# Optimization experiments

Hardware: AMD Instinct MI355X
Metric: run time of the kernel (lower is better)

## Reference

```python
import jax, jax.numpy as jnp
import numpy as np

B, N, M, D, H, F = 2, 2048, 2048, 512, 8, 2048
EPS = 1e-6


def _ln(x, g, b):
    mu = x.mean(-1, keepdims=True)
    var = ((x - mu) ** 2).mean(-1, keepdims=True)
    return (x - mu) / jnp.sqrt(var + EPS) * g + b


def setup_inputs() -> dict:
    key = jax.random.key(0)
    ks = jax.random.split(key, 12)
    g = lambda k, s: (jax.random.normal(k, s, jnp.float32) * 0.02)
    inp = {
        "x": jax.random.normal(ks[0], (B, N, D), jnp.float32),
        "y": jax.random.normal(ks[1], (B, M, D), jnp.float32),
        "mask_x": jnp.ones((B, N), jnp.float32),
        "mask_y": jnp.ones((B, M), jnp.float32),
        # MaskAttention params (weights stored as [in, out], applied as x @ W + b)
        "Wq": g(ks[2], (D, D)), "bq": jnp.zeros((D,), jnp.float32),
        "Wk": g(ks[3], (D, D)), "bk": jnp.zeros((D,), jnp.float32),
        "Wv": g(ks[4], (D, D)), "bv": jnp.zeros((D,), jnp.float32),
        "Wo": g(ks[5], (D, D)), "bo": jnp.zeros((D,), jnp.float32),
        # Mlp params
        "W1": g(ks[6], (D, F)), "b1": g(ks[7], (F,)) * 1e-4,
        "W2": g(ks[8], (F, D)), "b2": g(ks[9], (D,)) * 1e-4,
        # LayerNorm params (attention_norm shared between x and y; ffn_norm)
        "ln1_g": jnp.ones((D,), jnp.float32), "ln1_b": jnp.zeros((D,), jnp.float32),
        "ln2_g": jnp.ones((D,), jnp.float32), "ln2_b": jnp.zeros((D,), jnp.float32),
    }
    return inp


def reference(x, y, mask_x, mask_y, Wq, bq, Wk, bk, Wv, bv, Wo, bo,
              W1, b1, W2, b2, ln1_g, ln1_b, ln2_g, ln2_b):
    b, n, d = x.shape
    dh = d // H
    h = x
    xn = _ln(x, ln1_g, ln1_b)   # shared attention_norm
    yn = _ln(y, ln1_g, ln1_b)
    # masked Q/K/V projections (mask applied to mixed layers before head split)
    q = (xn @ Wq + bq) * mask_x[..., None]
    k = (yn @ Wk + bk) * mask_y[..., None]
    v = (yn @ Wv + bv) * mask_y[..., None]
    q = q.reshape(b, n, H, dh)
    k = k.reshape(b, -1, H, dh)
    v = v.reshape(b, -1, H, dh)
    scores = jnp.einsum("bnhd,bmhd->bhnm", q, k) / np.sqrt(dh)  # [B,H,N,M]
    probs = jax.nn.softmax(scores, axis=-1)
    ctx = jnp.einsum("bhnm,bmhd->bnhd", probs, v).reshape(b, n, d)
    attn_out = ctx @ Wo + bo  # proj_dropout is identity in eval
    x = h + attn_out
    h2 = x
    xn2 = _ln(x, ln2_g, ln2_b)
    ff = jax.nn.gelu(xn2 @ W1 + b1, approximate=False) @ W2 + b2
    return h2 + ff
```

## Files before the change

### kernel.cpp

```cpp
#include <hip/hip_runtime.h>
#include <hip/hip_bf16.h>

#define B_  2
#define N_  2048
#define M_  2048
#define D_  512
#define H_  8
#define F_  2048
#define DH_ 64
#define ROWS 4096

#define SPLIT 4
#define KV_PER (M_ / SPLIT)
#define NT (KV_PER / 64)

typedef __bf16 bf16x8 __attribute__((ext_vector_type(8)));
typedef __bf16 bf16x4v __attribute__((ext_vector_type(4)));
typedef float  f32x4  __attribute__((ext_vector_type(4)));
using bf16 = __hip_bfloat16;

__global__ __launch_bounds__(256) void ln_kernel(
    const float* __restrict__ in, const float* __restrict__ gam,
    const float* __restrict__ bet, bf16* __restrict__ out)
{
    int wave = threadIdx.x >> 6, lane = threadIdx.x & 63;
    int row  = blockIdx.x * 4 + wave;
    const float* p = in + (size_t)row * D_ + lane * 8;
    float4 v0 = *(const float4*)p;
    float4 v1 = *(const float4*)(p + 4);
    float s  = v0.x + v0.y + v0.z + v0.w + v1.x + v1.y + v1.z + v1.w;
    float ss = v0.x*v0.x + v0.y*v0.y + v0.z*v0.z + v0.w*v0.w
             + v1.x*v1.x + v1.y*v1.y + v1.z*v1.z + v1.w*v1.w;
    for (int m = 1; m < 64; m <<= 1) {
        s  += __shfl_xor(s,  m, 64);
        ss += __shfl_xor(ss, m, 64);
    }
    float mu   = s * (1.f / D_);
    float var  = ss * (1.f / D_) - mu * mu;
    float rstd = rsqrtf(var + 1e-6f);
    int c = lane * 8;
    float4 g0 = *(const float4*)(gam + c), g1 = *(const float4*)(gam + c + 4);
    float4 b0 = *(const float4*)(bet + c), b1 = *(const float4*)(bet + c + 4);
    bf16* o = out + (size_t)row * D_ + c;
    o[0] = __float2bfloat16((v0.x - mu) * rstd * g0.x + b0.x);
    o[1] = __float2bfloat16((v0.y - mu) * rstd * g0.y + b0.y);
    o[2] = __float2bfloat16((v0.z - mu) * rstd * g0.z + b0.z);
    o[3] = __float2bfloat16((v0.w - mu) * rstd * g0.w + b0.w);
    o[4] = __float2bfloat16((v1.x - mu) * rstd * g1.x + b1.x);
    o[5] = __float2bfloat16((v1.y - mu) * rstd * g1.y + b1.y);
    o[6] = __float2bfloat16((v1.z - mu) * rstd * g1.z + b1.z);
    o[7] = __float2bfloat16((v1.w - mu) * rstd * g1.w + b1.w);
}

__global__ void wtrans_kernel(const float* __restrict__ W, bf16* __restrict__ Wt,
                              int K, int N)
{
    __shared__ float t[32][33];
    int tx = threadIdx.x, ty = threadIdx.y;
    int n0 = blockIdx.x * 32, k0 = blockIdx.y * 32;
    for (int j = 0; j < 32; j += 8)
        t[ty + j][tx] = W[(size_t)(k0 + ty + j) * N + n0 + tx];
    __syncthreads();
    for (int j = 0; j < 32; j += 8)
        Wt[(size_t)(n0 + ty + j) * K + k0 + tx] = __float2bfloat16(t[tx][ty + j]);
}

__global__ void wtrans4_kernel(const float* __restrict__ Wq, const float* __restrict__ Wk,
                               const float* __restrict__ Wv, const float* __restrict__ Wo,
                               bf16* __restrict__ Wqt, bf16* __restrict__ Wkt,
                               bf16* __restrict__ Wvt, bf16* __restrict__ Wot)
{
    int z = blockIdx.z;
    const float* W = z == 0 ? Wq : (z == 1 ? Wk : (z == 2 ? Wv : Wo));
    bf16* Wt       = z == 0 ? Wqt : (z == 1 ? Wkt : (z == 2 ? Wvt : Wot));
    __shared__ float t[32][33];
    int tx = threadIdx.x, ty = threadIdx.y;
    int n0 = blockIdx.x * 32, k0 = blockIdx.y * 32;
    for (int j = 0; j < 32; j += 8)
        t[ty + j][tx] = W[(size_t)(k0 + ty + j) * D_ + n0 + tx];
    __syncthreads();
    for (int j = 0; j < 32; j += 8)
        Wt[(size_t)(n0 + ty + j) * D_ + k0 + tx] = __float2bfloat16(t[tx][ty + j]);
}

__global__ void vtrans_kernel(const bf16* __restrict__ v, bf16* __restrict__ vt)
{
    __shared__ bf16 t[32][33];
    int tx = threadIdx.x, ty = threadIdx.y;
    int bh = blockIdx.z, b = bh >> 3, h = bh & 7;
    int m0 = blockIdx.x * 32, d0 = blockIdx.y * 32;
    for (int j = 0; j < 32; j += 8)
        t[ty + j][tx] = v[(size_t)(b * M_ + m0 + ty + j) * D_ + h * DH_ + d0 + tx];
    __syncthreads();
    for (int j = 0; j < 32; j += 8)
        vt[((size_t)bh * DH_ + d0 + ty + j) * M_ + m0 + tx] = t[tx][ty + j];
}

#define BM 128
#define BN 128
#define BK 32
#define LDK 40

#define GEMM_BODY(Aptr, Btptr, KK, EPILOGUE)                                         \
    __shared__ bf16 As[BM * LDK];                                                    \
    __shared__ bf16 Bs[BN * LDK];                                                    \
    int t = threadIdx.x;                                                             \
    int lane = t & 63, wave = t >> 6;                                                \
    int wm = wave >> 1, wn = wave & 1;                                               \
    int r16 = lane & 15, g = lane >> 4;                                              \
    int m0 = blockIdx.x * BM, n0 = blockIdx.y * BN;                                  \
    f32x4 acc[4][4] = {};                                                            \
    for (int k0 = 0; k0 < (KK); k0 += BK) {                                          \
        __syncthreads();                                                             \
        for (int it = 0; it < 2; ++it) {                                             \
            int c = it * 256 + t;                                                    \
            int row = c >> 2, ko = (c & 3) * 8;                                      \
            uint4 dA = *(const uint4*)((Aptr)  + (size_t)(m0 + row) * (KK) + k0 + ko); \
            *(uint4*)((char*)As + row * (LDK * 2) + ko * 2) = dA;                    \
            uint4 dB = *(const uint4*)((Btptr) + (size_t)(n0 + row) * (KK) + k0 + ko); \
            *(uint4*)((char*)Bs + row * (LDK * 2) + ko * 2) = dB;                    \
        }                                                                            \
        __syncthreads();                                                             \
        bf16x8 af[4], bfr[4];                                                        \
        for (int i = 0; i < 4; ++i)                                                  \
            af[i]  = *(const bf16x8*)((char*)As + (wm * 64 + i * 16 + r16) * (LDK * 2) + g * 16); \
        for (int i = 0; i < 4; ++i)                                                  \
            bfr[i] = *(const bf16x8*)((char*)Bs + (wn * 64 + i * 16 + r16) * (LDK * 2) + g * 16); \
        for (int i = 0; i < 4; ++i)                                                  \
            for (int j = 0; j < 4; ++j)                                              \
                acc[i][j] = __builtin_amdgcn_mfma_f32_16x16x32_bf16(af[i], bfr[j], acc[i][j], 0, 0, 0); \
    }                                                                                \
    for (int i = 0; i < 4; ++i) {                                                    \
        int rb = m0 + wm * 64 + i * 16 + g * 4;                                      \
        for (int j = 0; j < 4; ++j) {                                                \
            int cb = n0 + wn * 64 + j * 16 + r16;                                    \
            float bia = bias[cb];                                                    \
            for (int e = 0; e < 4; ++e) {                                            \
                int rr = rb + e;                                                     \
                float val = acc[i][j][e] + bia;                                      \
                EPILOGUE                                                             \
            }                                                                        \
        }                                                                            \
    }

template<bool GELU, bool RESID, bool ROWMASK, bool OUTBF>
__global__ __launch_bounds__(256) void gemm_bt(
    const bf16* __restrict__ A, const bf16* __restrict__ Bt,
    const float* __restrict__ bias, const float* __restrict__ resid,
    const float* __restrict__ rowmask,
    bf16* __restrict__ outb, float* __restrict__ outf,
    int Mr, int Nn, int K)
{
    GEMM_BODY(A, Bt, K,
        if (GELU)    val = 0.5f * val * (1.f + erff(val * 0.70710678118654752f));
        if (RESID)   val += resid[(size_t)rr * Nn + cb];
        if (ROWMASK) val *= rowmask[rr];
        if (OUTBF)   outb[(size_t)rr * Nn + cb] = __float2bfloat16(val);
        else         outf[(size_t)rr * Nn + cb] = val;
    )
}

template<bool RESID, bool ROWMASK, bool OUTBF>
__device__ __forceinline__ void gemm64_body(
    const bf16* __restrict__ A, const bf16* __restrict__ Bt,
    const float* __restrict__ bias, const float* __restrict__ resid,
    const float* __restrict__ rowmask,
    bf16* __restrict__ outb, float* __restrict__ outf,
    int Nn, int K)
{
    __shared__ __align__(16) char As[2][64 * 128];
    __shared__ __align__(16) char Bs[2][64 * 128];
    int t = threadIdx.x, lane = t & 63, wave = t >> 6;
    int wm = wave >> 1, wn = wave & 1;
    int r16 = lane & 15, g = lane >> 4;
    int m0 = blockIdx.x * 64, n0 = blockIdx.y * 64;

    const int sr0 = t >> 3, sr1 = sr0 + 32, sc = t & 7;
    const int wof0 = sr0 * 128 + ((sc ^ (sr0 & 7)) << 4);
    const int wof1 = sr1 * 128 + ((sc ^ (sr1 & 7)) << 4);
    const int rsw0 = ((g     ^ (r16 & 7)) << 4);
    const int rsw1 = (((4 + g) ^ (r16 & 7)) << 4);

    uint4 a0, a1, b0, b1;
#define G64_LOAD(k0)                                                         \
    a0 = *(const uint4*)(A  + (size_t)(m0 + sr0) * K + (k0) + sc * 8);       \
    a1 = *(const uint4*)(A  + (size_t)(m0 + sr1) * K + (k0) + sc * 8);       \
    b0 = *(const uint4*)(Bt + (size_t)(n0 + sr0) * K + (k0) + sc * 8);       \
    b1 = *(const uint4*)(Bt + (size_t)(n0 + sr1) * K + (k0) + sc * 8);
#define G64_WRITE(buf)                                                       \
    *(uint4*)(As[buf] + wof0) = a0;  *(uint4*)(As[buf] + wof1) = a1;         \
    *(uint4*)(Bs[buf] + wof0) = b0;  *(uint4*)(Bs[buf] + wof1) = b1;

    f32x4 acc[2][2] = {};
    G64_LOAD(0)
    G64_WRITE(0)
    int cur = 0;
    const int nit = K >> 6;
    for (int it = 0; it < nit; ++it) {
        if (it + 1 < nit) { G64_LOAD((it + 1) << 6) }
        __syncthreads();
        bf16x8 af[2][2], bfr[2][2];
#pragma unroll
        for (int i = 0; i < 2; ++i) {
            af[i][0] = *(const bf16x8*)(As[cur] + (wm * 32 + i * 16 + r16) * 128 + rsw0);
            af[i][1] = *(const bf16x8*)(As[cur] + (wm * 32 + i * 16 + r16) * 128 + rsw1);
            bfr[i][0] = *(const bf16x8*)(Bs[cur] + (wn * 32 + i * 16 + r16) * 128 + rsw0);
            bfr[i][1] = *(const bf16x8*)(Bs[cur] + (wn * 32 + i * 16 + r16) * 128 + rsw1);
        }
        __builtin_amdgcn_s_setprio(1);
#pragma unroll
        for (int i = 0; i < 2; ++i)
#pragma unroll
            for (int j = 0; j < 2; ++j) {
                acc[i][j] = __builtin_amdgcn_mfma_f32_16x16x32_bf16(af[i][0], bfr[j][0], acc[i][j], 0, 0, 0);
                acc[i][j] = __builtin_amdgcn_mfma_f32_16x16x32_bf16(af[i][1], bfr[j][1], acc[i][j], 0, 0, 0);
            }
        __builtin_amdgcn_s_setprio(0);
        if (it + 1 < nit) { G64_WRITE(cur ^ 1) }
        cur ^= 1;
    }
#undef G64_LOAD
#undef G64_WRITE

#pragma unroll
    for (int i = 0; i < 2; ++i) {
        int rb = m0 + wm * 32 + i * 16 + g * 4;
#pragma unroll
        for (int j = 0; j < 2; ++j) {
            int cb = n0 + wn * 32 + j * 16 + r16;
            float bia = bias[cb];
#pragma unroll
            for (int e = 0; e < 4; ++e) {
                int rr = rb + e;
                float val = acc[i][j][e] + bia;
                if (RESID)   val += resid[(size_t)rr * Nn + cb];
                if (ROWMASK) val *= rowmask[rr];
                if (OUTBF)   outb[(size_t)rr * Nn + cb] = __float2bfloat16(val);
                else         outf[(size_t)rr * Nn + cb] = val;
            }
        }
    }
}

template<bool RESID, bool OUTBF>
__global__ __launch_bounds__(256) void gemm64(
    const bf16* __restrict__ A, const bf16* __restrict__ Bt,
    const float* __restrict__ bias, const float* __restrict__ resid,
    bf16* __restrict__ outb, float* __restrict__ outf, int Nn, int K)
{
    gemm64_body<RESID, false, OUTBF>(A, Bt, bias, resid, nullptr, outb, outf, Nn, K);
}

__global__ __launch_bounds__(256) void gemm64_qkv(
    const bf16* __restrict__ xn, const bf16* __restrict__ yn,
    const bf16* __restrict__ Wqt, const bf16* __restrict__ Wkt, const bf16* __restrict__ Wvt,
    const float* __restrict__ bq, const float* __restrict__ bk, const float* __restrict__ bv,
    const float* __restrict__ mask_x, const float* __restrict__ mask_y,
    bf16* __restrict__ qb, bf16* __restrict__ kb, bf16* __restrict__ vb)
{
    int z = blockIdx.z;
    const bf16* A        = z == 0 ? xn : yn;
    const bf16* Bt       = z == 0 ? Wqt : (z == 1 ? Wkt : Wvt);
    const float* bias    = z == 0 ? bq  : (z == 1 ? bk  : bv);
    const float* rowmask = z == 0 ? mask_x : mask_y;
    bf16* outb           = z == 0 ? qb  : (z == 1 ? kb  : vb);
    gemm64_body<false, true, true>(A, Bt, bias, nullptr, rowmask, outb, nullptr, D_, D_);
}

__global__ __launch_bounds__(256, 3) void attn_kernel(
    const bf16* __restrict__ q, const bf16* __restrict__ kk,
    const bf16* __restrict__ vt, float* __restrict__ num,
    float* __restrict__ ml)
{
    int bh = blockIdx.y, b = bh >> 3, h = bh & 7;
    int n0 = blockIdx.x * 128;
    int sp = blockIdx.z;
    int t = threadIdx.x, lane = t & 63, wave = t >> 6;
    int ql = lane & 15, gg = lane >> 4;

    __shared__ __align__(16) char KsB[2][64 * 128];
    __shared__ __align__(16) char VsB[2][64 * 128];
    __shared__ __align__(16) bf16 plds[4][16][72];

    bf16x8 qf0[2], qf1[2];
    {
        int qr0 = b * N_ + n0 + wave * 32 + ql;
        for (int ks = 0; ks < 2; ++ks) {
            bf16x8 qv = *(const bf16x8*)(q + (size_t)qr0 * D_ + h * DH_ + ks * 32 + gg * 8);
            for (int j = 0; j < 8; ++j) qv[j] = (__bf16)((float)qv[j] * 0.125f);
            qf0[ks] = qv;
            bf16x8 qw = *(const bf16x8*)(q + (size_t)(qr0 + 16) * D_ + h * DH_ + ks * 32 + gg * 8);
            for (int j = 0; j < 8; ++j) qw[j] = (__bf16)((float)qw[j] * 0.125f);
            qf1[ks] = qw;
        }
    }

    f32x4 cacc0[4] = {}, cacc1[4] = {};
    float m0r = -1e30f, l0r = 0.f, m1r = -1e30f, l1r = 0.f;

    const bf16* kbase = kk + (size_t)(b * M_ + sp * KV_PER) * D_ + h * DH_;
    const bf16* vtb   = vt + (size_t)bh * DH_ * M_ + sp * KV_PER;

    const int k0r = t >> 3,          kc0 = t & 7;
    const int k1r = (t >> 3) + 32;
    const int wofs0 = k0r * 128 + ((kc0 ^ (k0r & 7)) << 4);
    const int wofs1 = k1r * 128 + ((kc0 ^ (k1r & 7)) << 4);
    const int rsw0 = ((gg     ^ (ql & 7)) << 4);
    const int rsw1 = (((4 + gg) ^ (ql & 7)) << 4);

#define STAGE_LOAD(tt)                                                              \
    kw0 = *(const uint4*)(kbase + (size_t)((tt) * 64 + k0r) * D_ + kc0 * 8);        \
    kw1 = *(const uint4*)(kbase + (size_t)((tt) * 64 + k1r) * D_ + kc0 * 8);        \
    vw0 = *(const uint4*)(vtb + (size_t)k0r * M_ + (tt) * 64 + kc0 * 8);            \
    vw1 = *(const uint4*)(vtb + (size_t)k1r * M_ + (tt) * 64 + kc0 * 8);

#define STAGE_WRITE(buf)                                                            \
    *(uint4*)(KsB[buf] + wofs0) = kw0;                                              \
    *(uint4*)(KsB[buf] + wofs1) = kw1;                                              \
    *(uint4*)(VsB[buf] + wofs0) = vw0;                                              \
    *(uint4*)(VsB[buf] + wofs1) = vw1;

#define SOFTMAX_PV(S, MR, LR, CACC)                                                 \
    {                                                                               \
        float tmax = fmaxf(                                                         \
            fmaxf(fmaxf(fmaxf(S[0][0], S[0][1]), fmaxf(S[0][2], S[0][3])),          \
                  fmaxf(fmaxf(S[1][0], S[1][1]), fmaxf(S[1][2], S[1][3]))),         \
            fmaxf(fmaxf(fmaxf(S[2][0], S[2][1]), fmaxf(S[2][2], S[2][3])),          \
                  fmaxf(fmaxf(S[3][0], S[3][1]), fmaxf(S[3][2], S[3][3]))));        \
        tmax = fmaxf(tmax, __shfl_xor(tmax, 16, 64));                               \
        tmax = fmaxf(tmax, __shfl_xor(tmax, 32, 64));                               \
        float mnew = fmaxf(MR, tmax);                                               \
        float scl  = __expf(MR - mnew);                                             \
        MR = mnew;                                                                  \
        float p[4][4]; float ps = 0.f;                                              \
        for (int nf = 0; nf < 4; ++nf)                                              \
            for (int e = 0; e < 4; ++e) { p[nf][e] = __expf(S[nf][e] - mnew); ps += p[nf][e]; } \
        ps += __shfl_xor(ps, 16, 64);                                               \
        ps += __shfl_xor(ps, 32, 64);                                               \
        LR = LR * scl + ps;                                                         \
        for (int df = 0; df < 4; ++df)                                              \
            for (int e = 0; e < 4; ++e) CACC[df][e] *= scl;                         \
        for (int nf = 0; nf < 4; ++nf) {                                            \
            bf16x4v w;                                                              \
            w[0] = (__bf16)p[nf][0]; w[1] = (__bf16)p[nf][1];                       \
            w[2] = (__bf16)p[nf][2]; w[3] = (__bf16)p[nf][3];                       \
            *(bf16x4v*)(&plds[wave][ql][nf * 16 + 4 * gg]) = w;                     \
        }                                                                           \
        __builtin_amdgcn_s_setprio(1);                                              \
        for (int ks = 0; ks < 2; ++ks) {                                            \
            bf16x8 pf = *(const bf16x8*)((const char*)&plds[wave][0][0]             \
                                         + ql * 144 + ks * 64 + gg * 16);           \
            for (int df = 0; df < 4; ++df)                                          \
                CACC[df] = __builtin_amdgcn_mfma_f32_16x16x32_bf16(                 \
                    vf[df * 2 + ks], pf, CACC[df], 0, 0, 0);                        \
        }                                                                           \
        __builtin_amdgcn_s_setprio(0);                                              \
    }

    uint4 kw0, kw1, vw0, vw1;
    STAGE_LOAD(0)
    STAGE_WRITE(0)
    int cur = 0;

    for (int tt = 0; tt < NT; ++tt) {
        if (tt + 1 < NT) { STAGE_LOAD(tt + 1) }
        __syncthreads();

        const char* Kb = KsB[cur];
        const char* Vb = VsB[cur];

        bf16x8 kf[8];
#pragma unroll
        for (int nf = 0; nf < 4; ++nf) {
            kf[nf * 2 + 0] = *(const bf16x8*)(Kb + (nf * 16 + ql) * 128 + rsw0);
            kf[nf * 2 + 1] = *(const bf16x8*)(Kb + (nf * 16 + ql) * 128 + rsw1);
        }

        f32x4 s0[4] = {}, s1[4] = {};
        __builtin_amdgcn_s_setprio(1);
#pragma unroll
        for (int nf = 0; nf < 4; ++nf) {
            s0[nf] = __builtin_amdgcn_mfma_f32_16x16x32_bf16(kf[nf * 2 + 0], qf0[0], s0[nf], 0, 0, 0);
            s0[nf] = __builtin_amdgcn_mfma_f32_16x16x32_bf16(kf[nf * 2 + 1], qf0[1], s0[nf], 0, 0, 0);
            s1[nf] = __builtin_amdgcn_mfma_f32_16x16x32_bf16(kf[nf * 2 + 0], qf1[0], s1[nf], 0, 0, 0);
            s1[nf] = __builtin_amdgcn_mfma_f32_16x16x32_bf16(kf[nf * 2 + 1], qf1[1], s1[nf], 0, 0, 0);
        }
        __builtin_amdgcn_s_setprio(0);

        bf16x8 vf[8];
#pragma unroll
        for (int df = 0; df < 4; ++df) {
            vf[df * 2 + 0] = *(const bf16x8*)(Vb + (df * 16 + ql) * 128 + rsw0);
            vf[df * 2 + 1] = *(const bf16x8*)(Vb + (df * 16 + ql) * 128 + rsw1);
        }

        SOFTMAX_PV(s0, m0r, l0r, cacc0)
        SOFTMAX_PV(s1, m1r, l1r, cacc1)

        if (tt + 1 < NT) { STAGE_WRITE(cur ^ 1) }
        cur ^= 1;
    }

    {
        int qr0 = b * N_ + n0 + wave * 32 + ql;
        float* nb0 = num + (size_t)sp * ROWS * D_ + (size_t)qr0 * D_ + h * DH_;
        float* nb1 = num + (size_t)sp * ROWS * D_ + (size_t)(qr0 + 16) * D_ + h * DH_;
#pragma unroll
        for (int df = 0; df < 4; ++df) {
            *(f32x4*)(nb0 + df * 16 + 4 * gg) = cacc0[df];
            *(f32x4*)(nb1 + df * 16 + 4 * gg) = cacc1[df];
        }
        if (lane < 16) {
            size_t base = ((size_t)(sp * (B_ * H_) + bh) * N_ + (n0 + wave * 32 + ql)) * 2;
            ml[base] = m0r; ml[base + 1] = l0r;
            size_t base1 = ((size_t)(sp * (B_ * H_) + bh) * N_ + (n0 + wave * 32 + 16 + ql)) * 2;
            ml[base1] = m1r; ml[base1 + 1] = l1r;
        }
    }
#undef STAGE_LOAD
#undef STAGE_WRITE
#undef SOFTMAX_PV
}

__global__ __launch_bounds__(256) void attn_combine(
    const float* __restrict__ num, const float* __restrict__ ml,
    bf16* __restrict__ ctx)
{
    int idx = blockIdx.x * 256 + threadIdx.x;
    int row = idx >> 7;
    int c4  = (idx & 127) << 2;
    int b = row >> 11, n = row & (N_ - 1);
    int h = c4 >> 6;
    int bh = (b << 3) + h;
    float mv[SPLIT], lv[SPLIT];
#pragma unroll
    for (int sp = 0; sp < SPLIT; ++sp) {
        const float* mp = ml + ((size_t)(sp * (B_ * H_) + bh) * N_ + n) * 2;
        mv[sp] = mp[0]; lv[sp] = mp[1];
    }
    float mx = mv[0];
#pragma unroll
    for (int sp = 1; sp < SPLIT; ++sp) mx = fmaxf(mx, mv[sp]);
    float den = 0.f;
    float wsc[SPLIT];
#pragma unroll
    for (int sp = 0; sp < SPLIT; ++sp) {
        wsc[sp] = __expf(mv[sp] - mx);
        den += wsc[sp] * lv[sp];
    }
    float inv = 1.f / den;
    float ax = 0.f, ay = 0.f, az = 0.f, aw = 0.f;
#pragma unroll
    for (int sp = 0; sp < SPLIT; ++sp) {
        float4 v = *(const float4*)(num + (size_t)sp * ROWS * D_ + (size_t)row * D_ + c4);
        ax += wsc[sp] * v.x; ay += wsc[sp] * v.y;
        az += wsc[sp] * v.z; aw += wsc[sp] * v.w;
    }
    bf16* o = ctx + (size_t)row * D_ + c4;
    o[0] = __float2bfloat16(ax * inv);
    o[1] = __float2bfloat16(ay * inv);
    o[2] = __float2bfloat16(az * inv);
    o[3] = __float2bfloat16(aw * inv);
}

extern "C" void kernel_launch(void* const* d_in, const int* in_sizes, int n_in,
                              void* d_out, int out_size, void* d_ws, size_t ws_size,
                              hipStream_t stream)
{
    const float* x      = (const float*)d_in[0];
    const float* y      = (const float*)d_in[1];
    const float* mask_x = (const float*)d_in[2];
    const float* mask_y = (const float*)d_in[3];
    const float* Wq = (const float*)d_in[4];  const float* bq = (const float*)d_in[5];
    const float* Wk = (const float*)d_in[6];  const float* bk = (const float*)d_in[7];
    const float* Wv = (const float*)d_in[8];  const float* bv = (const float*)d_in[9];
    const float* Wo = (const float*)d_in[10]; const float* bo = (const float*)d_in[11];
    const float* W1 = (const float*)d_in[12]; const float* b1 = (const float*)d_in[13];
    const float* W2 = (const float*)d_in[14]; const float* b2 = (const float*)d_in[15];
    const float* ln1g = (const float*)d_in[16]; const float* ln1b = (const float*)d_in[17];
    const float* ln2g = (const float*)d_in[18]; const float* ln2b = (const float*)d_in[19];

    char* ws = (char*)d_ws;
    const size_t SZA = (size_t)ROWS * D_ * 2;
    bf16* xn   = (bf16*)ws;            ws += SZA;
    bf16* yn   = (bf16*)ws;            ws += SZA;
    bf16* qb   = (bf16*)ws;            ws += SZA;
    bf16* kb   = (bf16*)ws;            ws += SZA;
    bf16* vb   = (bf16*)ws;            ws += SZA;
    bf16* vtb  = (bf16*)ws;            ws += SZA;
    bf16* ctxb = (bf16*)ws;            ws += SZA;
    bf16* xn2  = (bf16*)ws;            ws += SZA;
    bf16* hff  = (bf16*)ws;            ws += (size_t)ROWS * F_ * 2;
    float* x1  = (float*)ws;           ws += (size_t)ROWS * D_ * 4;
    bf16* Wqt = (bf16*)ws;             ws += (size_t)D_ * D_ * 2;
    bf16* Wkt = (bf16*)ws;             ws += (size_t)D_ * D_ * 2;
    bf16* Wvt = (bf16*)ws;             ws += (size_t)D_ * D_ * 2;
    bf16* Wot = (bf16*)ws;             ws += (size_t)D_ * D_ * 2;
    bf16* W1t = (bf16*)ws;             ws += (size_t)D_ * F_ * 2;
    bf16* W2t = (bf16*)ws;             ws += (size_t)F_ * D_ * 2;
    float* num = (float*)ws;           ws += (size_t)SPLIT * ROWS * D_ * 4;
    float* mlb = (float*)ws;           ws += (size_t)SPLIT * B_ * H_ * N_ * 2 * 4;

    dim3 tb(32, 8);
    wtrans4_kernel<<<dim3(D_ / 32, D_ / 32, 4), tb, 0, stream>>>(
        Wq, Wk, Wv, Wo, Wqt, Wkt, Wvt, Wot);
    wtrans_kernel<<<dim3(F_ / 32, D_ / 32), tb, 0, stream>>>(W1, W1t, D_, F_);
    wtrans_kernel<<<dim3(D_ / 32, F_ / 32), tb, 0, stream>>>(W2, W2t, F_, D_);

    ln_kernel<<<ROWS / 4, 256, 0, stream>>>(x, ln1g, ln1b, xn);
    ln_kernel<<<ROWS / 4, 256, 0, stream>>>(y, ln1g, ln1b, yn);

    gemm64_qkv<<<dim3(ROWS / 64, D_ / 64, 3), 256, 0, stream>>>(
        xn, yn, Wqt, Wkt, Wvt, bq, bk, bv, mask_x, mask_y, qb, kb, vb);

    vtrans_kernel<<<dim3(M_ / 32, DH_ / 32, B_ * H_), tb, 0, stream>>>(vb, vtb);

    attn_kernel<<<dim3(N_ / 128, B_ * H_, SPLIT), 256, 0, stream>>>(qb, kb, vtb, num, mlb);
    attn_combine<<<(ROWS * D_ / 4) / 256, 256, 0, stream>>>(num, mlb, ctxb);

    gemm64<true, false><<<dim3(ROWS / 64, D_ / 64), 256, 0, stream>>>(
        ctxb, Wot, bo, x, nullptr, x1, D_, D_);

    ln_kernel<<<ROWS / 4, 256, 0, stream>>>(x1, ln2g, ln2b, xn2);

    gemm_bt<true, false, false, true><<<dim3(ROWS / BM, F_ / BN), 256, 0, stream>>>(
        xn2, W1t, b1, nullptr, nullptr, hff, nullptr, ROWS, F_, D_);

    gemm64<true, false><<<dim3(ROWS / 64, D_ / 64), 256, 0, stream>>>(
        hff, W2t, b2, x1, nullptr, (float*)d_out, D_, F_);
}
```

Baseline: 137.1 us.

## Halve attention split, remap grid for XCD locality, lazy rescale, bf16 partials

Reduces the KV split from 4 to 2 and flattens the attention grid to 1D, remapping block IDs so consecutive blocks are spread across the 8 XCDs in a locality-friendly order. The online softmax now rescales the accumulator and running max only when some lane's tile max exceeds the stored max by more than 8, skipping the exp and multiplies in most iterations. Partial numerators are stored as bf16 instead of fp32, halving combine traffic. The risks are less parallelism with fewer splits, an extra rounding step on the partials, and probabilities that can exceed 1 (up to e^8) before normalisation, which loosens precision.

```diff
diff --git a/kernel.cpp b/kernel.cpp
--- a/kernel.cpp
+++ b/kernel.cpp
@@ -10,9 +10,10 @@
 #define DH_ 64
 #define ROWS 4096
 
-#define SPLIT 4
+#define SPLIT 2
 #define KV_PER (M_ / SPLIT)
 #define NT (KV_PER / 64)
+#define ATT_GRID (16 * 16 * SPLIT)
 
 typedef __bf16 bf16x8 __attribute__((ext_vector_type(8)));
 typedef __bf16 bf16x4v __attribute__((ext_vector_type(4)));
@@ -269,12 +270,15 @@
 
 __global__ __launch_bounds__(256, 3) void attn_kernel(
     const bf16* __restrict__ q, const bf16* __restrict__ kk,
-    const bf16* __restrict__ vt, float* __restrict__ num,
+    const bf16* __restrict__ vt, bf16* __restrict__ num,
     float* __restrict__ ml)
 {
-    int bh = blockIdx.y, b = bh >> 3, h = bh & 7;
-    int n0 = blockIdx.x * 128;
-    int sp = blockIdx.z;
+    int bid = blockIdx.x;
+    int wg  = (bid & 7) * (ATT_GRID / 8) + (bid >> 3);
+    int n0  = (wg & 15) * 128;
+    int bh  = (wg >> 4) & 15;
+    int sp  = wg >> 8;
+    int b = bh >> 3, h = bh & 7;
     int t = threadIdx.x, lane = t & 63, wave = t >> 6;
     int ql = lane & 15, gg = lane >> 4;
 
@@ -329,17 +333,20 @@
                   fmaxf(fmaxf(S[3][0], S[3][1]), fmaxf(S[3][2], S[3][3]))));        \
         tmax = fmaxf(tmax, __shfl_xor(tmax, 16, 64));                               \
         tmax = fmaxf(tmax, __shfl_xor(tmax, 32, 64));                               \
-        float mnew = fmaxf(MR, tmax);                                               \
-        float scl  = __expf(MR - mnew);                                             \
-        MR = mnew;                                                                  \
+        if (__any(tmax - MR > 8.f)) {                     \
+            float mnew = fmaxf(MR, tmax);                                           \
+            float scl  = __expf(MR - mnew);                                         \
+            MR = mnew;                                                              \
+            LR *= scl;                                                              \
+            for (int df = 0; df < 4; ++df)                                          \
+                for (int e = 0; e < 4; ++e) CACC[df][e] *= scl;                     \
+        }                                                                           \
         float p[4][4]; float ps = 0.f;                                              \
         for (int nf = 0; nf < 4; ++nf)                                              \
-            for (int e = 0; e < 4; ++e) { p[nf][e] = __expf(S[nf][e] - mnew); ps += p[nf][e]; } \
+            for (int e = 0; e < 4; ++e) { p[nf][e] = __expf(S[nf][e] - MR); ps += p[nf][e]; } \
         ps += __shfl_xor(ps, 16, 64);                                               \
         ps += __shfl_xor(ps, 32, 64);                                               \
-        LR = LR * scl + ps;                                                         \
-        for (int df = 0; df < 4; ++df)                                              \
-            for (int e = 0; e < 4; ++e) CACC[df][e] *= scl;                         \
+        LR += ps;                                                                   \
         for (int nf = 0; nf < 4; ++nf) {                                            \
             bf16x4v w;                                                              \
             w[0] = (__bf16)p[nf][0]; w[1] = (__bf16)p[nf][1];                       \
@@ -403,12 +410,18 @@
 
     {
         int qr0 = b * N_ + n0 + wave * 32 + ql;
-        float* nb0 = num + (size_t)sp * ROWS * D_ + (size_t)qr0 * D_ + h * DH_;
-        float* nb1 = num + (size_t)sp * ROWS * D_ + (size_t)(qr0 + 16) * D_ + h * DH_;
+        bf16* nb0 = num + (size_t)sp * ROWS * D_ + (size_t)qr0 * D_ + h * DH_;
+        bf16* nb1 = num + (size_t)sp * ROWS * D_ + (size_t)(qr0 + 16) * D_ + h * DH_;
 #pragma unroll
         for (int df = 0; df < 4; ++df) {
-            *(f32x4*)(nb0 + df * 16 + 4 * gg) = cacc0[df];
-            *(f32x4*)(nb1 + df * 16 + 4 * gg) = cacc1[df];
+            bf16x4v w0, w1;
+#pragma unroll
+            for (int e = 0; e < 4; ++e) {
+                w0[e] = (__bf16)cacc0[df][e];
+                w1[e] = (__bf16)cacc1[df][e];
+            }
+            *(bf16x4v*)(nb0 + df * 16 + 4 * gg) = w0;
+            *(bf16x4v*)(nb1 + df * 16 + 4 * gg) = w1;
         }
         if (lane < 16) {
             size_t base = ((size_t)(sp * (B_ * H_) + bh) * N_ + (n0 + wave * 32 + ql)) * 2;
@@ -423,7 +436,7 @@
 }
 
 __global__ __launch_bounds__(256) void attn_combine(
-    const float* __restrict__ num, const float* __restrict__ ml,
+    const bf16* __restrict__ num, const float* __restrict__ ml,
     bf16* __restrict__ ctx)
 {
     int idx = blockIdx.x * 256 + threadIdx.x;
@@ -452,9 +465,9 @@
     float ax = 0.f, ay = 0.f, az = 0.f, aw = 0.f;
 #pragma unroll
     for (int sp = 0; sp < SPLIT; ++sp) {
-        float4 v = *(const float4*)(num + (size_t)sp * ROWS * D_ + (size_t)row * D_ + c4);
-        ax += wsc[sp] * v.x; ay += wsc[sp] * v.y;
-        az += wsc[sp] * v.z; aw += wsc[sp] * v.w;
+        bf16x4v v = *(const bf16x4v*)(num + (size_t)sp * ROWS * D_ + (size_t)row * D_ + c4);
+        ax += wsc[sp] * (float)v[0]; ay += wsc[sp] * (float)v[1];
+        az += wsc[sp] * (float)v[2]; aw += wsc[sp] * (float)v[3];
     }
     bf16* o = ctx + (size_t)row * D_ + c4;
     o[0] = __float2bfloat16(ax * inv);
@@ -498,7 +511,7 @@
     bf16* Wot = (bf16*)ws;             ws += (size_t)D_ * D_ * 2;
     bf16* W1t = (bf16*)ws;             ws += (size_t)D_ * F_ * 2;
     bf16* W2t = (bf16*)ws;             ws += (size_t)F_ * D_ * 2;
-    float* num = (float*)ws;           ws += (size_t)SPLIT * ROWS * D_ * 4;
+    bf16* numb = (bf16*)ws;            ws += (size_t)SPLIT * ROWS * D_ * 2;
     float* mlb = (float*)ws;           ws += (size_t)SPLIT * B_ * H_ * N_ * 2 * 4;
 
     dim3 tb(32, 8);
@@ -515,8 +528,8 @@
 
     vtrans_kernel<<<dim3(M_ / 32, DH_ / 32, B_ * H_), tb, 0, stream>>>(vb, vtb);
 
-    attn_kernel<<<dim3(N_ / 128, B_ * H_, SPLIT), 256, 0, stream>>>(qb, kb, vtb, num, mlb);
-    attn_combine<<<(ROWS * D_ / 4) / 256, 256, 0, stream>>>(num, mlb, ctxb);
+    attn_kernel<<<ATT_GRID, 256, 0, stream>>>(qb, kb, vtb, numb, mlb);
+    attn_combine<<<(ROWS * D_ / 4) / 256, 256, 0, stream>>>(numb, mlb, ctxb);
 
     gemm64<true, false><<<dim3(ROWS / 64, D_ / 64), 256, 0, stream>>>(
         ctxb, Wot, bo, x, nullptr, x1, D_, D_);
```

Measured after the change: 126.1 us. 8.0% less time.
